# Kernel tuning notes

Measured on AMD Instinct MI355X. Metric: run time of the kernel, lower is better.

## Reference

```python
import jax, jax.numpy as jnp
import numpy as np

N_NODES = 100000
N_EDGES = 1000000
NUM_GRAPHS = 100
EPS_BN = 1e-5
EPS_GATE = 1e-6


def _bn(x, gamma, beta):
    # BatchNorm1d in training mode: batch statistics over dim 0
    mu = jnp.mean(x, axis=0)
    var = jnp.var(x, axis=0)
    return (x - mu) * jax.lax.rsqrt(var + EPS_BN) * gamma + beta


def _gated_gcn_layer(h, e, snorm_n, snorm_e, W, b, g_h, b_h, g_e, b_e, src, dst):
    # W: [5, d, d] stacking A, B, C, D, E projections; b: [5, d]
    Ah = h @ W[0] + b[0]
    Bh = h @ W[1] + b[1]
    Ce = e @ W[2] + b[2]
    Dh = h @ W[3] + b[3]
    Eh = h @ W[4] + b[4]
    # edge update: e_ji = Dh_src + Eh_dst + Ce   [E, d]
    e_new = Dh[src] + Eh[dst] + Ce
    sigma = jax.nn.sigmoid(e_new)
    # node update: gated sum of source messages at destination nodes
    num = jax.ops.segment_sum(sigma * Bh[src], dst, num_segments=h.shape[0])
    den = jax.ops.segment_sum(sigma, dst, num_segments=h.shape[0])
    h_new = Ah + num / (den + EPS_GATE)
    # graph size normalization
    h_new = h_new * snorm_n
    e_new = e_new * snorm_e
    # batch norm + relu + residual (dropout = 0.0)
    h_new = jax.nn.relu(_bn(h_new, g_h, b_h))
    e_new = jax.nn.relu(_bn(e_new, g_e, b_e))
    return h + h_new, e + e_new


def setup_inputs() -> dict:
    key = jax.random.key(0)
    ks = jax.random.split(key, 12)
    nodes_feat = jax.random.normal(ks[0], (N_NODES, 64), jnp.float32)
    edges_feat = jax.random.normal(ks[1], (N_EDGES, 1), jnp.float32)
    snorm_n = jax.random.uniform(ks[2], (N_NODES, 1), jnp.float32)
    snorm_e = jax.random.uniform(ks[3], (N_EDGES, 1), jnp.float32)
    src = jax.random.randint(ks[4], (N_EDGES,), 0, N_NODES, jnp.int32)
    dst = jax.random.randint(ks[5], (N_EDGES,), 0, N_NODES, jnp.int32)
    node_graph_ids = jnp.sort(jax.random.randint(ks[6], (N_NODES,), 0, NUM_GRAPHS, jnp.int32))
    Wh = jax.random.normal(ks[7], (64, 70), jnp.float32) * 0.1
    bh = jnp.zeros((70,), jnp.float32)
    We = jax.random.normal(ks[8], (1, 70), jnp.float32) * 0.1
    be = jnp.zeros((70,), jnp.float32)
    W_gcn = jax.random.normal(ks[9], (3, 5, 70, 70), jnp.float32) * 0.1
    b_gcn = jnp.zeros((3, 5, 70), jnp.float32)
    bn_gamma_h = jnp.ones((3, 70), jnp.float32)
    bn_beta_h = jnp.zeros((3, 70), jnp.float32)
    bn_gamma_e = jnp.ones((3, 70), jnp.float32)
    bn_beta_e = jnp.zeros((3, 70), jnp.float32)
    return {"nodes_feat": nodes_feat, "edges_feat": edges_feat, "snorm_n": snorm_n,
            "snorm_e": snorm_e, "src": src, "dst": dst, "node_graph_ids": node_graph_ids,
            "Wh": Wh, "bh": bh, "We": We, "be": be, "W_gcn": W_gcn, "b_gcn": b_gcn,
            "bn_gamma_h": bn_gamma_h, "bn_beta_h": bn_beta_h,
            "bn_gamma_e": bn_gamma_e, "bn_beta_e": bn_beta_e}


def reference(nodes_feat, edges_feat, snorm_n, snorm_e, src, dst, node_graph_ids,
              Wh, bh, We, be, W_gcn, b_gcn, bn_gamma_h, bn_beta_h, bn_gamma_e, bn_beta_e):
    h = nodes_feat @ Wh + bh
    e = edges_feat @ We + be
    # hidden_dims = [70, 70] -> only gated_gcn_1 (params index 0) and gated_gcn_o (index 2)
    for li in (0, 2):
        h, e = _gated_gcn_layer(h, e, snorm_n, snorm_e, W_gcn[li], b_gcn[li],
                                bn_gamma_h[li], bn_beta_h[li], bn_gamma_e[li], bn_beta_e[li],
                                src, dst)
    # dgl.mean_nodes: per-graph mean of node features
    sums = jax.ops.segment_sum(h, node_graph_ids, num_segments=NUM_GRAPHS)
    counts = jax.ops.segment_sum(jnp.ones((h.shape[0],), h.dtype), node_graph_ids,
                                 num_segments=NUM_GRAPHS)
    hg = sums / jnp.maximum(counts, 1.0)[:, None]
    return hg
```

## Files before the change

### kernel.cpp

```cpp
#include <hip/hip_runtime.h>

#define NN 100000
#define NE 1000000
#define NG 100
#define DD 70
#define EL0 64
#define CH0 (9 * EL0)
#define TPW 5
#define EPW (16 * TPW)
#define EPB (4 * EPW)
#define SCB 512
#define WTS (70 * 72)

typedef __attribute__((ext_vector_type(8))) short bf16x8;
typedef __attribute__((ext_vector_type(4))) float f32x4;

__device__ __forceinline__ float sigmoidf_(float x) { return 1.f / (1.f + expf(-x)); }

__device__ __forceinline__ unsigned int rne_bf16(float x) {
    unsigned int u = __float_as_uint(x);
    return (u + 0x7FFFu + ((u >> 16) & 1u)) >> 16;
}
__device__ __forceinline__ float b2f(unsigned short u) {
    return __uint_as_float(((unsigned int)u) << 16);
}
__device__ __forceinline__ float lo2f(unsigned int u) { return __uint_as_float(u << 16); }
__device__ __forceinline__ float hi2f(unsigned int u) { return __uint_as_float(u & 0xFFFF0000u); }

#define DOT4(acc, vv, ww) { acc = fmaf((vv).x, (ww).x, acc); acc = fmaf((vv).y, (ww).y, acc); \
                            acc = fmaf((vv).z, (ww).z, acc); acc = fmaf((vv).w, (ww).w, acc); }

__global__ void k_trAll(const float* __restrict__ Wh, const float* __restrict__ Wg,
                        float* __restrict__ WT) {
    int m = blockIdx.y, f = blockIdx.x, k = threadIdx.x;
    const float* W;
    int K = DD;
    switch (m) {
        case 0: W = Wh; K = 64; break;
        case 1: W = Wg + 0 * 4900; break;
        case 2: W = Wg + 1 * 4900; break;
        case 3: W = Wg + 3 * 4900; break;
        case 4: W = Wg + 4 * 4900; break;
        case 5: W = Wg + 10 * 4900; break;
        case 6: W = Wg + 11 * 4900; break;
        case 7: W = Wg + 13 * 4900; break;
        default: W = Wg + 14 * 4900; break;
    }
    if (k < 72) WT[(m * 70 + f) * 72 + k] = (k < K) ? W[k * DD + f] : 0.f;
}

__global__ __launch_bounds__(640) void k_dense_r(const float* __restrict__ x, int K,
                                                 const float* __restrict__ WTm,
                                                 const float* __restrict__ bias,
                                                 float* __restrict__ out, int nrows) {
    __shared__ float sx[36 * 72];
    int t = threadIdx.x;
    int r = t / DD, f = t - r * DD;
    long rb = (long)blockIdx.x * 36;
    for (int idx = t; idx < 36 * 72; idx += 640) {
        int rr = idx / 72, kk = idx - rr * 72;
        long i = rb + rr;
        sx[idx] = (kk < K && i < nrows) ? x[i * K + kk] : 0.f;
    }
    __syncthreads();
    if (r < 9) {
        const float4* wr = (const float4*)(WTm + f * 72);
        float bb = bias[f];
        float a0 = bb, a1 = bb, a2 = bb, a3 = bb;
        const float4* s0 = (const float4*)&sx[(r) * 72];
        const float4* s1 = (const float4*)&sx[(r + 9) * 72];
        const float4* s2 = (const float4*)&sx[(r + 18) * 72];
        const float4* s3 = (const float4*)&sx[(r + 27) * 72];
#pragma unroll 1
        for (int q = 0; q < 18; q += 2) {
            float4 wA = wr[q], wB = wr[q + 1];
            float4 vA0 = s0[q], vB0 = s0[q + 1];
            DOT4(a0, vA0, wA) DOT4(a0, vB0, wB)
            float4 vA1 = s1[q], vB1 = s1[q + 1];
            DOT4(a1, vA1, wA) DOT4(a1, vB1, wB)
            float4 vA2 = s2[q], vB2 = s2[q + 1];
            DOT4(a2, vA2, wA) DOT4(a2, vB2, wB)
            float4 vA3 = s3[q], vB3 = s3[q + 1];
            DOT4(a3, vA3, wA) DOT4(a3, vB3, wB)
        }
        long i0 = rb + r, i1 = i0 + 9, i2 = i0 + 18, i3 = i0 + 27;
        if (i0 < nrows) out[i0 * DD + f] = a0;
        if (i1 < nrows) out[i1 * DD + f] = a1;
        if (i2 < nrows) out[i2 * DD + f] = a2;
        if (i3 < nrows) out[i3 * DD + f] = a3;
    }
}

#define PROJ(MIDX, BIAS, STORE)                                                   \
    {                                                                             \
        const float4* wr = (const float4*)(WT4 + (MIDX) * WTS + f * 72);          \
        float bb = (BIAS)[f];                                                     \
        float a0 = bb, a1 = bb, a2 = bb, a3 = bb;                                 \
        _Pragma("unroll 1")                                                       \
        for (int q = 0; q < 18; q += 2) {                                         \
            float4 wA = wr[q], wB = wr[q + 1];                                    \
            float4 vA0 = s0[q], vB0 = s0[q + 1];                                  \
            DOT4(a0, vA0, wA) DOT4(a0, vB0, wB)                                   \
            float4 vA1 = s1[q], vB1 = s1[q + 1];                                  \
            DOT4(a1, vA1, wA) DOT4(a1, vB1, wB)                                   \
            float4 vA2 = s2[q], vB2 = s2[q + 1];                                  \
            DOT4(a2, vA2, wA) DOT4(a2, vB2, wB)                                   \
            float4 vA3 = s3[q], vB3 = s3[q + 1];                                  \
            DOT4(a3, vA3, wA) DOT4(a3, vB3, wB)                                   \
        }                                                                         \
        STORE(0, i0, a0)                                                          \
        STORE(1, i1, a1)                                                          \
        STORE(2, i2, a2)                                                          \
        STORE(3, i3, a3)                                                          \
    }

__global__ __launch_bounds__(640) void k_dense_q(
    const float* __restrict__ x, const float* __restrict__ WT4,
    const float* __restrict__ bA, const float* __restrict__ bB,
    const float* __restrict__ bD, const float* __restrict__ bE,
    float* __restrict__ outA, unsigned short* __restrict__ outDstd,
    unsigned short* __restrict__ outE, unsigned int* __restrict__ outDB, int nrows) {
    __shared__ float sx[36 * 72];
    int t = threadIdx.x;
    int r = t / DD, f = t - r * DD;
    long rb = (long)blockIdx.x * 36;
    for (int idx = t; idx < 36 * 72; idx += 640) {
        int rr = idx / 72, kk = idx - rr * 72;
        long i = rb + rr;
        sx[idx] = (kk < DD && i < nrows) ? x[i * DD + kk] : 0.f;
    }
    __syncthreads();
    if (r < 9) {
        const float4* s0 = (const float4*)&sx[(r) * 72];
        const float4* s1 = (const float4*)&sx[(r + 9) * 72];
        const float4* s2 = (const float4*)&sx[(r + 18) * 72];
        const float4* s3 = (const float4*)&sx[(r + 27) * 72];
        long i0 = rb + r, i1 = i0 + 9, i2 = i0 + 18, i3 = i0 + 27;
        float vB0 = 0.f, vB1 = 0.f, vB2 = 0.f, vB3 = 0.f;
#define ST_A(row, ii, aa) if ((ii) < nrows) outA[(ii) * DD + f] = (aa);
#define ST_B(row, ii, aa) vB##row = (aa);
#define ST_D(row, ii, aa) if ((ii) < nrows) { unsigned int ud = rne_bf16(aa); \
            outDstd[(ii) * DD + f] = (unsigned short)ud; \
            outDB[(ii) * DD + f] = ud | (rne_bf16(vB##row) << 16); }
#define ST_E(row, ii, aa) if ((ii) < nrows) outE[(ii) * DD + f] = (unsigned short)rne_bf16(aa);
        PROJ(0, bA, ST_A)
        PROJ(1, bB, ST_B)
        PROJ(2, bD, ST_D)
        PROJ(3, bE, ST_E)
#undef ST_A
#undef ST_B
#undef ST_D
#undef ST_E
    }
}

__global__ void k_pre(const float* __restrict__ We, const float* __restrict__ be,
                      const float* __restrict__ Wg, const float* __restrict__ bg,
                      float* __restrict__ v1, float* __restrict__ v2) {
    int f = threadIdx.x;
    if (f < DD) {
        const float* W2 = Wg + 2 * DD * DD;
        const float* b2 = bg + 2 * DD;
        float a = 0.f, c = 0.f;
        for (int k = 0; k < DD; ++k) {
            a = fmaf(We[k], W2[k * DD + f], a);
            c = fmaf(be[k], W2[k * DD + f], c);
        }
        v1[f] = a;
        v2[f] = c + b2[f];
    }
}

__global__ void k_prep2(const float* __restrict__ v1, const float* __restrict__ v2,
                        const float* __restrict__ murs_e, const float* __restrict__ ge,
                        const float* __restrict__ bbe, const float* __restrict__ We,
                        const float* __restrict__ be, const float* __restrict__ Wg,
                        float* __restrict__ CT2, unsigned short* __restrict__ WB) {
    int t = threadIdx.x;
    if (t < 35) {
        int f0 = 2 * t, f1 = 2 * t + 1;
        float A0 = murs_e[DD + f0] * ge[f0], A1 = murs_e[DD + f1] * ge[f1];
        float* c = CT2 + t * 12;
        c[0] = v1[f0];  c[1] = v1[f1];
        c[2] = v2[f0];  c[3] = v2[f1];
        c[4] = A0;      c[5] = A1;
        c[6] = bbe[f0] - murs_e[f0] * A0;
        c[7] = bbe[f1] - murs_e[f1] * A1;
        c[8] = We[f0];  c[9] = We[f1];
        c[10] = be[f0]; c[11] = be[f1];
    }
    const float* WC2 = Wg + 12 * 4900;
    for (int idx = t; idx < 960; idx += 512) {
        int nt = idx / 192, rem = idx - nt * 192;
        int c = rem / 64, l = rem - c * 64;
        int n = nt * 16 + (l & 15);
        int kb = c * 32 + (l >> 4) * 8;
        for (int j = 0; j < 8; ++j) {
            int k = kb + j;
            unsigned short v = 0;
            if (k < 70 && n < 70) v = (unsigned short)rne_bf16(WC2[k * 70 + n]);
            WB[((nt * 3 + c) * 64 + l) * 8 + j] = v;
        }
    }
}

__global__ void k_count(const int* __restrict__ dst, int* __restrict__ off) {
    int j = blockIdx.x * 256 + threadIdx.x;
    if (j < NE) atomicAdd(&off[dst[j]], 1);
}

__global__ void k_scan_a(int* __restrict__ off, int* __restrict__ part) {
    __shared__ int s[SCB];
    int t = threadIdx.x, i = blockIdx.x * SCB + t;
    int v = (i < NN) ? off[i] : 0;
    s[t] = v;
    __syncthreads();
    for (int d = 1; d < SCB; d <<= 1) {
        int x = (t >= d) ? s[t - d] : 0;
        __syncthreads();
        s[t] += x;
        __syncthreads();
    }
    if (i < NN) off[i] = s[t] - v;
    if (t == SCB - 1) part[blockIdx.x] = s[t];
}

__global__ void k_scan_b(int* __restrict__ part, int nb) {
    __shared__ int s[256];
    int t = threadIdx.x;
    int v = (t < nb) ? part[t] : 0;
    s[t] = v;
    __syncthreads();
    for (int d = 1; d < 256; d <<= 1) {
        int x = (t >= d) ? s[t - d] : 0;
        __syncthreads();
        s[t] += x;
        __syncthreads();
    }
    if (t < nb) part[t] = s[t] - v;
}

__global__ void k_scan_c(int* __restrict__ off, const int* __restrict__ part) {
    int i = blockIdx.x * SCB + threadIdx.x;
    if (i < NN) off[i] += part[blockIdx.x];
}

__global__ void k_fill(const int* __restrict__ src, const int* __restrict__ dst,
                       const float* __restrict__ ef, const float* __restrict__ sne,
                       int* __restrict__ off, int* __restrict__ src_s,
                       float* __restrict__ ef_s, float* __restrict__ sne_s,
                       int* __restrict__ dst_s) {
    int j = blockIdx.x * 256 + threadIdx.x;
    if (j < NE) {
        int d = dst[j];
        int pos = atomicAdd(&off[d], 1);
        src_s[pos] = src[j];
        ef_s[pos] = ef[j];
        sne_s[pos] = sne[j];
        dst_s[pos] = d;
    }
}

__global__ __launch_bounds__(640) void k_edge0(
    const float* __restrict__ ef_s, const float* __restrict__ sne_s,
    const int* __restrict__ src_s, const int* __restrict__ dst_s,
    const unsigned int* __restrict__ DB0, const unsigned short* __restrict__ PE,
    const float* __restrict__ v1, const float* __restrict__ v2,
    float* __restrict__ num, float* __restrict__ den, float* __restrict__ red) {
    int t = threadIdx.x;
    int r = t / DD, f = t - r * DD;
    bool act = (r < 9);
    float c1 = 0.f, c2 = 0.f;
    if (act) { c1 = v1[f]; c2 = v2[f]; }
    float acc_s = 0.f, acc_q = 0.f;
    int e_beg = blockIdx.x * CH0 + r * EL0;
    bool live = act && e_beg < NE;
    int dcur = 0;
    float pe = 0.f, accn = 0.f, accd = 0.f;
    int lim = 0;
    if (live) {
        dcur = dst_s[e_beg];
        pe = b2f(PE[(long)dcur * DD + f]);
        lim = NE - e_beg;
        if (lim > EL0) lim = EL0;
    }
    for (int g = 0; g < lim; g += 4) {
        int m = lim - g;
        if (m > 4) m = 4;
        int dj[4];
        unsigned int dbj[4];
        float efj[4], snj[4];
#pragma unroll
        for (int j = 0; j < 4; ++j) {
            if (j < m) {
                int e = e_beg + g + j;
                int s = src_s[e];
                dj[j] = dst_s[e];
                efj[j] = ef_s[e];
                snj[j] = sne_s[e];
                dbj[j] = DB0[(long)s * DD + f];
            }
        }
#pragma unroll
        for (int j = 0; j < 4; ++j) {
            if (j < m) {
                if (dj[j] != dcur) {
                    unsafeAtomicAdd(&num[(long)dcur * DD + f], accn);
                    unsafeAtomicAdd(&den[(long)dcur * DD + f], accd);
                    accn = 0.f; accd = 0.f;
                    dcur = dj[j];
                    pe = b2f(PE[(long)dcur * DD + f]);
                }
                float en = lo2f(dbj[j]) + pe + efj[j] * c1 + c2;
                float sg = sigmoidf_(en);
                accn = fmaf(sg, hi2f(dbj[j]), accn);
                accd += sg;
                float tv = en * snj[j];
                acc_s += tv;
                acc_q = fmaf(tv, tv, acc_q);
            }
        }
    }
    if (live) {
        unsafeAtomicAdd(&num[(long)dcur * DD + f], accn);
        unsafeAtomicAdd(&den[(long)dcur * DD + f], accd);
    }
    __shared__ float ss[DD], sq[DD];
    if (t < DD) { ss[t] = 0.f; sq[t] = 0.f; }
    __syncthreads();
    if (act) { atomicAdd(&ss[f], acc_s); atomicAdd(&sq[f], acc_q); }
    __syncthreads();
    if (t < DD) {
        atomicAdd(&red[t], ss[t]);
        atomicAdd(&red[DD + t], sq[t]);
    }
}

__global__ __launch_bounds__(256) void k_edge2(
    const float* __restrict__ ef_s, const float* __restrict__ sne_s,
    const int* __restrict__ src_s, const int* __restrict__ dst_s,
    const unsigned short* __restrict__ PD0, const unsigned short* __restrict__ PE0,
    const unsigned int* __restrict__ DB2, const unsigned short* __restrict__ PE2,
    const float* __restrict__ CT2, const unsigned short* __restrict__ WB,
    const float* __restrict__ bC2, float* __restrict__ num, float* __restrict__ den) {
    __shared__ __align__(16) unsigned short As[4 * 16 * 104];
    int t = threadIdx.x;
    int w = t >> 6, l = t & 63;
    unsigned short* Aw = &As[w * 1664];
    for (int i = l; i < 832; i += 64) ((unsigned int*)Aw)[i] = 0u;
    int wb_e = blockIdx.x * EPB + w * EPW;
    if (wb_e >= NE) return;
    int col = l & 15, hi = l >> 4;
    bf16x8 bfr[15];
#pragma unroll
    for (int q = 0; q < 15; ++q)
        bfr[q] = *(const bf16x8*)(WB + (q * 64 + l) * 8);
    float bc[5];
#pragma unroll
    for (int nt = 0; nt < 5; ++nt) bc[nt] = bC2[nt * 16 + col];
    int e0p = wb_e + hi * 4;
    if (e0p > NE - 1) e0p = NE - 1;
    int dcur = dst_s[e0p];
    float an[5], ad[5], pe2c[5];
#pragma unroll
    for (int nt = 0; nt < 5; ++nt) {
        an[nt] = 0.f; ad[nt] = 0.f;
        int nv = nt * 16 + col;
        pe2c[nt] = (nv < 70) ? b2f(PE2[(long)dcur * DD + nv]) : 0.f;
    }
    for (int tt = 0; tt < TPW; ++tt) {
        int et = wb_e + tt * 16;
        if (et >= NE) break;
        for (int i = l; i < 560; i += 64) {
            int el = i / 35, fp = i - el * 35, f = fp * 2;
            int e = et + el;
            unsigned int val = 0u;
            if (e < NE) {
                int s = src_s[e], d = dst_s[e];
                float efv = ef_s[e], sn = sne_s[e];
                const float* ct = CT2 + fp * 12;
                unsigned int upd = *(const unsigned int*)(PD0 + (long)s * DD + f);
                unsigned int upe = *(const unsigned int*)(PE0 + (long)d * DD + f);
                float pdx = lo2f(upd), pdy = hi2f(upd);
                float pex = lo2f(upe), pey = hi2f(upe);
                float en0a = pdx + pex + efv * ct[0] + ct[2];
                float en0b = pdy + pey + efv * ct[1] + ct[3];
                float ra = fmaxf(fmaf(en0a * sn, ct[4], ct[6]), 0.f);
                float rb = fmaxf(fmaf(en0b * sn, ct[5], ct[7]), 0.f);
                float e1a = fmaf(efv, ct[8], ct[10]) + ra;
                float e1b = fmaf(efv, ct[9], ct[11]) + rb;
                val = rne_bf16(e1a) | (rne_bf16(e1b) << 16);
            }
            ((unsigned int*)Aw)[(el * 104 + f) >> 1] = val;
        }
        bf16x8 af[3];
#pragma unroll
        for (int c = 0; c < 3; ++c)
            af[c] = *(const bf16x8*)(Aw + (l & 15) * 104 + c * 32 + hi * 8);
        f32x4 acc[5];
#pragma unroll
        for (int nt = 0; nt < 5; ++nt) {
            acc[nt] = (f32x4){0.f, 0.f, 0.f, 0.f};
#pragma unroll
            for (int c = 0; c < 3; ++c)
                acc[nt] = __builtin_amdgcn_mfma_f32_16x16x32_bf16(af[c], bfr[nt * 3 + c],
                                                                  acc[nt], 0, 0, 0);
        }
#pragma unroll
        for (int j = 0; j < 4; ++j) {
            int e = et + hi * 4 + j;
            if (e < NE) {
                int d = dst_s[e];
                if (d != dcur) {
#pragma unroll
                    for (int nt = 0; nt < 5; ++nt) {
                        int nv = nt * 16 + col;
                        if (nv < 70) {
                            unsafeAtomicAdd(&num[(long)dcur * DD + nv], an[nt]);
                            unsafeAtomicAdd(&den[(long)dcur * DD + nv], ad[nt]);
                        }
                        an[nt] = 0.f; ad[nt] = 0.f;
                    }
                    dcur = d;
#pragma unroll
                    for (int nt = 0; nt < 5; ++nt) {
                        int nv = nt * 16 + col;
                        if (nv < 70) pe2c[nt] = b2f(PE2[(long)dcur * DD + nv]);
                    }
                }
                int s = src_s[e];
#pragma unroll
                for (int nt = 0; nt < 5; ++nt) {
                    int nv = nt * 16 + col;
                    if (nv < 70) {
                        unsigned int db = DB2[(long)s * DD + nv];
                        float en = acc[nt][j] + bc[nt] + lo2f(db) + pe2c[nt];
                        float sg = sigmoidf_(en);
                        an[nt] = fmaf(sg, hi2f(db), an[nt]);
                        ad[nt] += sg;
                    }
                }
            }
        }
    }
#pragma unroll
    for (int nt = 0; nt < 5; ++nt) {
        int nv = nt * 16 + col;
        if (nv < 70) {
            unsafeAtomicAdd(&num[(long)dcur * DD + nv], an[nt]);
            unsafeAtomicAdd(&den[(long)dcur * DD + nv], ad[nt]);
        }
    }
}

__global__ __launch_bounds__(640) void k_nstats(const float* __restrict__ PA,
                                                const float* __restrict__ num,
                                                const float* __restrict__ den,
                                                const float* __restrict__ snn,
                                                float* __restrict__ red) {
    int t = threadIdx.x;
    int r = t / DD, f = t - r * DD;
    bool act = (r < 9);
    float acc_s = 0.f, acc_q = 0.f;
    const int T = (NN + 8) / 9;
    for (int tile = blockIdx.x; tile < T; tile += gridDim.x) {
        int i = tile * 9 + r;
        if (act && i < NN) {
            long o = (long)i * DD + f;
            float v = (PA[o] + num[o] / (den[o] + 1e-6f)) * snn[i];
            acc_s += v;
            acc_q = fmaf(v, v, acc_q);
        }
    }
    __shared__ float ss[DD], sq[DD];
    if (t < DD) { ss[t] = 0.f; sq[t] = 0.f; }
    __syncthreads();
    if (act) { atomicAdd(&ss[f], acc_s); atomicAdd(&sq[f], acc_q); }
    __syncthreads();
    if (t < DD) {
        atomicAdd(&red[t], ss[t]);
        atomicAdd(&red[DD + t], sq[t]);
    }
}

__global__ void k_stats(const float* __restrict__ sums, float* __restrict__ murs, float invn) {
    int f = threadIdx.x;
    if (f < DD) {
        float mu = sums[f] * invn;
        float var = sums[DD + f] * invn - mu * mu;
        murs[f] = mu;
        murs[DD + f] = rsqrtf(var + 1e-5f);
    }
}

__global__ __launch_bounds__(256) void k_apply(const float* __restrict__ hin,
                                               const float* __restrict__ PA,
                                               const float* __restrict__ num,
                                               const float* __restrict__ den,
                                               const float* __restrict__ snn,
                                               const float* __restrict__ murs,
                                               const float* __restrict__ g,
                                               const float* __restrict__ b,
                                               float* __restrict__ hout) {
    long idx = (long)blockIdx.x * 256 + threadIdx.x;
    if (idx < (long)NN * DD) {
        int i = (int)(idx / DD);
        int f = (int)(idx - (long)i * DD);
        float v = (PA[idx] + num[idx] / (den[idx] + 1e-6f)) * snn[i];
        float bnv = (v - murs[f]) * murs[DD + f] * g[f] + b[f];
        hout[idx] = hin[idx] + fmaxf(bnv, 0.f);
    }
}

__global__ __launch_bounds__(640) void k_readout(const float* __restrict__ h,
                                                 const int* __restrict__ gid,
                                                 float* __restrict__ gsum,
                                                 float* __restrict__ gcnt) {
    __shared__ float sv[9 * DD];
    __shared__ int sg_[9];
    int t = threadIdx.x;
    int r = t / DD, f = t - r * DD;
    int i = blockIdx.x * 9 + r;
    if (r < 9 && i < NN) {
        sv[r * DD + f] = h[(long)i * DD + f];
        if (f == 0) sg_[r] = gid[i];
    }
    __syncthreads();
    int nvalid = NN - blockIdx.x * 9;
    if (nvalid > 9) nvalid = 9;
    if (t < DD && nvalid > 0) {
        float acc = 0.f;
        int cur = sg_[0];
        for (int rr = 0; rr < nvalid; ++rr) {
            int g = sg_[rr];
            if (g != cur) {
                unsafeAtomicAdd(&gsum[cur * DD + t], acc);
                acc = 0.f;
                cur = g;
            }
            acc += sv[rr * DD + t];
        }
        unsafeAtomicAdd(&gsum[cur * DD + t], acc);
        if (t == 0) {
            int cnt = 0;
            cur = sg_[0];
            for (int rr = 0; rr < nvalid; ++rr) {
                if (sg_[rr] != cur) {
                    unsafeAtomicAdd(&gcnt[cur], (float)cnt);
                    cnt = 0;
                    cur = sg_[rr];
                }
                cnt++;
            }
            unsafeAtomicAdd(&gcnt[cur], (float)cnt);
        }
    }
}

__global__ void k_out(const float* __restrict__ gsum, const float* __restrict__ gcnt,
                      float* __restrict__ out) {
    int idx = blockIdx.x * 256 + threadIdx.x;
    if (idx < NG * DD) {
        int g = idx / DD;
        out[idx] = gsum[idx] / fmaxf(gcnt[g], 1.f);
    }
}

extern "C" void kernel_launch(void* const* d_in, const int* in_sizes, int n_in,
                              void* d_out, int out_size, void* d_ws, size_t ws_size,
                              hipStream_t stream) {
    const float* x   = (const float*)d_in[0];
    const float* ef  = (const float*)d_in[1];
    const float* snn = (const float*)d_in[2];
    const float* sne = (const float*)d_in[3];
    const int*   src = (const int*)d_in[4];
    const int*   dst = (const int*)d_in[5];
    const int*   gid = (const int*)d_in[6];
    const float* Wh  = (const float*)d_in[7];
    const float* bh  = (const float*)d_in[8];
    const float* We  = (const float*)d_in[9];
    const float* be  = (const float*)d_in[10];
    const float* Wg  = (const float*)d_in[11];
    const float* bg  = (const float*)d_in[12];
    const float* gh  = (const float*)d_in[13];
    const float* bbh = (const float*)d_in[14];
    const float* ge  = (const float*)d_in[15];
    const float* bbe = (const float*)d_in[16];
    float* out = (float*)d_out;

    const size_t NF = (size_t)NN * DD;

    float* ws = (float*)d_ws;
    float* B0 = ws;
    float* B1 = B0 + NF;
    float* B2 = B1 + NF;
    float* B3 = B2 + NF;
    float* B4 = B3 + NF;
    float* B5 = B4 + NF;
    float* B6 = B5 + NF;
    float* num = B6 + NF;
    float* den = num + NF;
    float* red  = den + NF;
    float* gsum = red + 4 * DD;
    float* gcnt = gsum + NG * DD;
    float* v1 = gcnt + NG;
    float* v2 = v1 + DD;
    float* murs_e = v2 + DD;
    float* murs_h = murs_e + 2 * DD;
    int* src_s = (int*)(murs_h + 2 * DD);
    float* ef_s  = (float*)(src_s + NE);
    float* sne_s = ef_s + NE;
    int* dst_s = (int*)(sne_s + NE);
    float* WT    = (float*)(dst_s + NE);
    uintptr_t pal = ((uintptr_t)(WT + 10 * WTS) + 15) & ~(uintptr_t)15;
    float* CT2 = (float*)pal;
    unsigned short* WB = (unsigned short*)(CT2 + 420);
    int* off  = (int*)num;
    int* part = off + NN;

    unsigned short* B3h = (unsigned short*)B3;
    unsigned short* B4h = (unsigned short*)B4;
    unsigned short* B5h = (unsigned short*)B5;
    unsigned short* B6h = (unsigned short*)B6;
    unsigned int*   B6u = (unsigned int*)B6;
    unsigned int*   B0u = (unsigned int*)B0;

    size_t need = (size_t)((char*)(WB + 7680) - (char*)d_ws);
    if (ws_size < need) return;

    const int NB_N36 = (NN + 35) / 36;
    const int NB_N9  = (NN + 8) / 9;
    const int NB_E256 = (NE + 255) / 256;
    const int NB_SC  = (NN + SCB - 1) / SCB;
    const int NB_E0  = (NE + CH0 - 1) / CH0;
    const int NB_E2  = (NE + EPB - 1) / EPB;

    hipMemsetAsync(off, 0, NN * sizeof(int), stream);
    k_trAll<<<dim3(70, 9), 72, 0, stream>>>(Wh, Wg, WT);
    k_count<<<NB_E256, 256, 0, stream>>>(dst, off);
    k_scan_a<<<NB_SC, SCB, 0, stream>>>(off, part);
    k_scan_b<<<1, 256, 0, stream>>>(part, NB_SC);
    k_scan_c<<<NB_SC, SCB, 0, stream>>>(off, part);
    k_fill<<<NB_E256, 256, 0, stream>>>(src, dst, ef, sne, off, src_s, ef_s, sne_s, dst_s);

    hipMemsetAsync(num, 0, (2 * NF + 4 * DD + NG * DD + NG) * sizeof(float), stream);

    k_pre<<<1, 128, 0, stream>>>(We, be, Wg, bg, v1, v2);
    k_dense_r<<<NB_N36, 640, 0, stream>>>(x, 64, WT + 0 * WTS, bh, B0, NN);

    k_dense_q<<<NB_N36, 640, 0, stream>>>(B0, WT + 1 * WTS, bg + 0 * 70, bg + 1 * 70,
                                          bg + 3 * 70, bg + 4 * 70, B2, B4h, B5h, B6u, NN);
    k_edge0<<<NB_E0, 640, 0, stream>>>(ef_s, sne_s, src_s, dst_s, B6u, B5h, v1, v2,
                                       num, den, red);
    k_stats<<<1, 128, 0, stream>>>(red, murs_e, 1.f / NE);
    k_prep2<<<1, 512, 0, stream>>>(v1, v2, murs_e, ge + 0, bbe + 0, We, be, Wg, CT2, WB);
    k_nstats<<<2048, 640, 0, stream>>>(B2, num, den, snn, red + 2 * DD);
    k_stats<<<1, 128, 0, stream>>>(red + 2 * DD, murs_h, 1.f / NN);
    k_apply<<<(int)((NF + 255) / 256), 256, 0, stream>>>(B0, B2, num, den, snn, murs_h,
                                                         gh + 0, bbh + 0, B1);

    hipMemsetAsync(num, 0, (2 * NF + 4 * DD) * sizeof(float), stream);
    k_dense_q<<<NB_N36, 640, 0, stream>>>(B1, WT + 5 * WTS, bg + 10 * 70, bg + 11 * 70,
                                          bg + 13 * 70, bg + 14 * 70, B2, B3h, B6h, B0u, NN);
    k_edge2<<<NB_E2, 256, 0, stream>>>(ef_s, sne_s, src_s, dst_s, B4h, B5h, B0u, B6h,
                                       CT2, WB, bg + 12 * 70, num, den);
    k_nstats<<<2048, 640, 0, stream>>>(B2, num, den, snn, red + 2 * DD);
    k_stats<<<1, 128, 0, stream>>>(red + 2 * DD, murs_h, 1.f / NN);
    k_apply<<<(int)((NF + 255) / 256), 256, 0, stream>>>(B1, B2, num, den, snn, murs_h,
                                                         gh + 2 * DD, bbh + 2 * DD, B1);

    k_readout<<<NB_N9, 640, 0, stream>>>(B1, gid, gsum, gcnt);
    k_out<<<(NG * DD + 255) / 256, 256, 0, stream>>>(gsum, gcnt, out);
}
```

Measured before the change: 1.583 ms.

## Remap edge0 threads to 16-lane feature groups and pair projections in dense_q

k_edge0 is remapped from one thread per (row, feature) in 640-thread blocks to 256-thread blocks. In each wave, 16 lanes cover the 70 features in five strided slots per thread, and four segments of 64 sorted edges are processed at once. The goal is fuller waves (no idle threads from 640 = 9*70+10) and coalesced 16-lane gathers, at the cost of less memory-level parallelism per thread since edges are now processed one at a time instead of batches of four. k_dense_q also computes two projections per pass so each shared-memory row load feeds both, at the price of more registers.

Result: no change. 1.565 ms, median of 2 (-1.2%).

```diff
diff --git a/kernel.cpp b/kernel.cpp
--- a/kernel.cpp
+++ b/kernel.cpp
@@ -4,8 +4,8 @@
 #define NE 1000000
 #define NG 100
 #define DD 70
-#define EL0 64
-#define CH0 (9 * EL0)
+#define SE0 64
+#define EPB0 (16 * SE0)
 #define TPW 5
 #define EPW (16 * TPW)
 #define EPB (4 * EPW)
@@ -91,27 +91,32 @@
     }
 }
 
-#define PROJ(MIDX, BIAS, STORE)                                                   \
+#define PROJ2(M0, M1, BIAS0, BIAS1, ST0, ST1)                                     \
     {                                                                             \
-        const float4* wr = (const float4*)(WT4 + (MIDX) * WTS + f * 72);          \
-        float bb = (BIAS)[f];                                                     \
-        float a0 = bb, a1 = bb, a2 = bb, a3 = bb;                                 \
+        const float4* wr0 = (const float4*)(WT4 + (M0) * WTS + f * 72);           \
+        const float4* wr1 = (const float4*)(WT4 + (M1) * WTS + f * 72);           \
+        float bb0 = (BIAS0)[f], bb1 = (BIAS1)[f];                                 \
+        float a0 = bb0, a1 = bb0, a2 = bb0, a3 = bb0;                             \
+        float c0 = bb1, c1 = bb1, c2 = bb1, c3 = bb1;                             \
         _Pragma("unroll 1")                                                       \
         for (int q = 0; q < 18; q += 2) {                                         \
-            float4 wA = wr[q], wB = wr[q + 1];                                    \
-            float4 vA0 = s0[q], vB0 = s0[q + 1];                                  \
-            DOT4(a0, vA0, wA) DOT4(a0, vB0, wB)                                   \
-            float4 vA1 = s1[q], vB1 = s1[q + 1];                                  \
-            DOT4(a1, vA1, wA) DOT4(a1, vB1, wB)                                   \
-            float4 vA2 = s2[q], vB2 = s2[q + 1];                                  \
-            DOT4(a2, vA2, wA) DOT4(a2, vB2, wB)                                   \
-            float4 vA3 = s3[q], vB3 = s3[q + 1];                                  \
-            DOT4(a3, vA3, wA) DOT4(a3, vB3, wB)                                   \
+            float4 wA0 = wr0[q], wB0 = wr0[q + 1];                                \
+            float4 wA1 = wr1[q], wB1 = wr1[q + 1];                                \
+            float4 vA = s0[q], vB = s0[q + 1];                                    \
+            DOT4(a0, vA, wA0) DOT4(a0, vB, wB0)                                   \
+            DOT4(c0, vA, wA1) DOT4(c0, vB, wB1)                                   \
+            vA = s1[q]; vB = s1[q + 1];                                           \
+            DOT4(a1, vA, wA0) DOT4(a1, vB, wB0)                                   \
+            DOT4(c1, vA, wA1) DOT4(c1, vB, wB1)                                   \
+            vA = s2[q]; vB = s2[q + 1];                                           \
+            DOT4(a2, vA, wA0) DOT4(a2, vB, wB0)                                   \
+            DOT4(c2, vA, wA1) DOT4(c2, vB, wB1)                                   \
+            vA = s3[q]; vB = s3[q + 1];                                           \
+            DOT4(a3, vA, wA0) DOT4(a3, vB, wB0)                                   \
+            DOT4(c3, vA, wA1) DOT4(c3, vB, wB1)                                   \
         }                                                                         \
-        STORE(0, i0, a0)                                                          \
-        STORE(1, i1, a1)                                                          \
-        STORE(2, i2, a2)                                                          \
-        STORE(3, i3, a3)                                                          \
+        ST0(0, i0, a0) ST0(1, i1, a1) ST0(2, i2, a2) ST0(3, i3, a3)               \
+        ST1(0, i0, c0) ST1(1, i1, c1) ST1(2, i2, c2) ST1(3, i3, c3)               \
     }
 
 __global__ __launch_bounds__(640) void k_dense_q(
@@ -143,10 +148,8 @@
             outDstd[(ii) * DD + f] = (unsigned short)ud; \
             outDB[(ii) * DD + f] = ud | (rne_bf16(vB##row) << 16); }
 #define ST_E(row, ii, aa) if ((ii) < nrows) outE[(ii) * DD + f] = (unsigned short)rne_bf16(aa);
-        PROJ(0, bA, ST_A)
-        PROJ(1, bB, ST_B)
-        PROJ(2, bD, ST_D)
-        PROJ(3, bE, ST_E)
+        PROJ2(0, 1, bA, bB, ST_A, ST_B)
+        PROJ2(2, 3, bD, bE, ST_D, ST_E)
 #undef ST_A
 #undef ST_B
 #undef ST_D
@@ -261,74 +264,87 @@
     }
 }
 
-__global__ __launch_bounds__(640) void k_edge0(
+__global__ __launch_bounds__(256) void k_edge0(
     const float* __restrict__ ef_s, const float* __restrict__ sne_s,
     const int* __restrict__ src_s, const int* __restrict__ dst_s,
     const unsigned int* __restrict__ DB0, const unsigned short* __restrict__ PE,
     const float* __restrict__ v1, const float* __restrict__ v2,
     float* __restrict__ num, float* __restrict__ den, float* __restrict__ red) {
-    int t = threadIdx.x;
-    int r = t / DD, f = t - r * DD;
-    bool act = (r < 9);
-    float c1 = 0.f, c2 = 0.f;
-    if (act) { c1 = v1[f]; c2 = v2[f]; }
-    float acc_s = 0.f, acc_q = 0.f;
-    int e_beg = blockIdx.x * CH0 + r * EL0;
-    bool live = act && e_beg < NE;
-    int dcur = 0;
-    float pe = 0.f, accn = 0.f, accd = 0.f;
-    int lim = 0;
+    __shared__ float ss[DD], sq[DD];
+    int t = threadIdx.x;
+    if (t < DD) { ss[t] = 0.f; sq[t] = 0.f; }
+    int w = t >> 6, l = t & 63;
+    int col = l & 15, hi = l >> 4;
+    float c1v[5], c2v[5];
+#pragma unroll
+    for (int nt = 0; nt < 5; ++nt) {
+        int nv = nt * 16 + col;
+        c1v[nt] = (nv < DD) ? v1[nv] : 0.f;
+        c2v[nt] = (nv < DD) ? v2[nv] : 0.f;
+    }
+    int e_beg = (blockIdx.x * 16 + w * 4 + hi) * SE0;
+    bool live = e_beg < NE;
+    int lim = live ? (NE - e_beg < SE0 ? NE - e_beg : SE0) : 0;
+    int dcur = live ? dst_s[e_beg] : 0;
+    float pec[5], an[5], ad[5], as_[5], aq[5];
+#pragma unroll
+    for (int nt = 0; nt < 5; ++nt) {
+        int nv = nt * 16 + col;
+        pec[nt] = (live && nv < DD) ? b2f(PE[(long)dcur * DD + nv]) : 0.f;
+        an[nt] = 0.f; ad[nt] = 0.f; as_[nt] = 0.f; aq[nt] = 0.f;
+    }
+    for (int ee = 0; ee < lim; ++ee) {
+        int e = e_beg + ee;
+        int d = dst_s[e], s = src_s[e];
+        float efv = ef_s[e], snv = sne_s[e];
+        if (d != dcur) {
+#pragma unroll
+            for (int nt = 0; nt < 5; ++nt) {
+                int nv = nt * 16 + col;
+                if (nv < DD) {
+                    unsafeAtomicAdd(&num[(long)dcur * DD + nv], an[nt]);
+                    unsafeAtomicAdd(&den[(long)dcur * DD + nv], ad[nt]);
+                }
+                an[nt] = 0.f; ad[nt] = 0.f;
+            }
+            dcur = d;
+#pragma unroll
+            for (int nt = 0; nt < 5; ++nt) {
+                int nv = nt * 16 + col;
+                if (nv < DD) pec[nt] = b2f(PE[(long)dcur * DD + nv]);
+            }
+        }
+#pragma unroll
+        for (int nt = 0; nt < 5; ++nt) {
+            int nv = nt * 16 + col;
+            if (nv < DD) {
+                unsigned int db = DB0[(long)s * DD + nv];
+                float en = lo2f(db) + pec[nt] + efv * c1v[nt] + c2v[nt];
+                float sg = sigmoidf_(en);
+                an[nt] = fmaf(sg, hi2f(db), an[nt]);
+                ad[nt] += sg;
+                float tv = en * snv;
+                as_[nt] += tv;
+                aq[nt] = fmaf(tv, tv, aq[nt]);
+            }
+        }
+    }
     if (live) {
-        dcur = dst_s[e_beg];
-        pe = b2f(PE[(long)dcur * DD + f]);
-        lim = NE - e_beg;
-        if (lim > EL0) lim = EL0;
-    }
-    for (int g = 0; g < lim; g += 4) {
-        int m = lim - g;
-        if (m > 4) m = 4;
-        int dj[4];
-        unsigned int dbj[4];
-        float efj[4], snj[4];
-#pragma unroll
-        for (int j = 0; j < 4; ++j) {
-            if (j < m) {
-                int e = e_beg + g + j;
-                int s = src_s[e];
-                dj[j] = dst_s[e];
-                efj[j] = ef_s[e];
-                snj[j] = sne_s[e];
-                dbj[j] = DB0[(long)s * DD + f];
-            }
-        }
-#pragma unroll
-        for (int j = 0; j < 4; ++j) {
-            if (j < m) {
-                if (dj[j] != dcur) {
-                    unsafeAtomicAdd(&num[(long)dcur * DD + f], accn);
-                    unsafeAtomicAdd(&den[(long)dcur * DD + f], accd);
-                    accn = 0.f; accd = 0.f;
-                    dcur = dj[j];
-                    pe = b2f(PE[(long)dcur * DD + f]);
-                }
-                float en = lo2f(dbj[j]) + pe + efj[j] * c1 + c2;
-                float sg = sigmoidf_(en);
-                accn = fmaf(sg, hi2f(dbj[j]), accn);
-                accd += sg;
-                float tv = en * snj[j];
-                acc_s += tv;
-                acc_q = fmaf(tv, tv, acc_q);
-            }
-        }
-    }
-    if (live) {
-        unsafeAtomicAdd(&num[(long)dcur * DD + f], accn);
-        unsafeAtomicAdd(&den[(long)dcur * DD + f], accd);
-    }
-    __shared__ float ss[DD], sq[DD];
-    if (t < DD) { ss[t] = 0.f; sq[t] = 0.f; }
-    __syncthreads();
-    if (act) { atomicAdd(&ss[f], acc_s); atomicAdd(&sq[f], acc_q); }
+#pragma unroll
+        for (int nt = 0; nt < 5; ++nt) {
+            int nv = nt * 16 + col;
+            if (nv < DD) {
+                unsafeAtomicAdd(&num[(long)dcur * DD + nv], an[nt]);
+                unsafeAtomicAdd(&den[(long)dcur * DD + nv], ad[nt]);
+            }
+        }
+    }
+    __syncthreads();
+#pragma unroll
+    for (int nt = 0; nt < 5; ++nt) {
+        int nv = nt * 16 + col;
+        if (nv < DD) { atomicAdd(&ss[nv], as_[nt]); atomicAdd(&sq[nv], aq[nt]); }
+    }
     __syncthreads();
     if (t < DD) {
         atomicAdd(&red[t], ss[t]);
@@ -632,7 +648,7 @@
     const int NB_N9  = (NN + 8) / 9;
     const int NB_E256 = (NE + 255) / 256;
     const int NB_SC  = (NN + SCB - 1) / SCB;
-    const int NB_E0  = (NE + CH0 - 1) / CH0;
+    const int NB_E0  = (NE + EPB0 - 1) / EPB0;
     const int NB_E2  = (NE + EPB - 1) / EPB;
 
     hipMemsetAsync(off, 0, NN * sizeof(int), stream);
@@ -650,7 +666,7 @@
 
     k_dense_q<<<NB_N36, 640, 0, stream>>>(B0, WT + 1 * WTS, bg + 0 * 70, bg + 1 * 70,
                                           bg + 3 * 70, bg + 4 * 70, B2, B4h, B5h, B6u, NN);
-    k_edge0<<<NB_E0, 640, 0, stream>>>(ef_s, sne_s, src_s, dst_s, B6u, B5h, v1, v2,
+    k_edge0<<<NB_E0, 256, 0, stream>>>(ef_s, sne_s, src_s, dst_s, B6u, B5h, v1, v2,
                                        num, den, red);
     k_stats<<<1, 128, 0, stream>>>(red, murs_e, 1.f / NE);
     k_prep2<<<1, 512, 0, stream>>>(v1, v2, murs_e, ge + 0, bbe + 0, We, be, Wg, CT2, WB);
```
